# Kernel tuning notes

Hardware: AMD Instinct MI355X
Metric: run time of the kernel (lower is better)

The kernel has to match this reference:

```python
import jax, jax.numpy as jnp
import numpy as np

B, S, D = 4, 2048, 1024
LN_EPS = 1e-3  # keras LayerNormalization default


def setup_inputs() -> dict:
    key = jax.random.key(0)
    ks = jax.random.split(key, 4)
    std = 1.0 / np.sqrt(D)
    return {
        "inputs": jax.random.normal(ks[0], (B, S, D), dtype=jnp.float32),
        "Wq": jax.random.normal(ks[1], (D, D), dtype=jnp.float32) * std,
        "bq": jnp.zeros((D,), jnp.float32),
        "Wk": jax.random.normal(ks[2], (D, D), dtype=jnp.float32) * std,
        "bk": jnp.zeros((D,), jnp.float32),
        "Wv": jax.random.normal(ks[3], (D, D), dtype=jnp.float32) * std,
        "bv": jnp.zeros((D,), jnp.float32),
        "ln_gamma": jnp.ones((D,), jnp.float32),
        "ln_beta": jnp.zeros((D,), jnp.float32),
    }


def reference(inputs, Wq, bq, Wk, bk, Wv, bv, ln_gamma, ln_beta):
    d = inputs.shape[-1]
    scale = jnp.sqrt(jnp.asarray(d, inputs.dtype))
    q = inputs @ Wq + bq          # [B,S,D]
    k = inputs @ Wk + bk
    v = inputs @ Wv + bv
    scores = jnp.einsum("bqd,bkd->bqk", q, k) / scale  # [B,S,S]
    attn = jax.nn.softmax(scores, axis=-1)
    context = jnp.einsum("bqk,bkd->bqd", attn, v)      # [B,S,D]
    resid = context + inputs
    mu = jnp.mean(resid, axis=-1, keepdims=True)
    var = jnp.mean(jnp.square(resid - mu), axis=-1, keepdims=True)
    normed = (resid - mu) * jax.lax.rsqrt(var + LN_EPS)
    return normed * ln_gamma + ln_beta
```

## Files before the change

kernel.cpp:

```cpp
#include <hip/hip_runtime.h>
#include <hip/hip_bf16.h>
#include <cstdint>
#include <cstddef>


typedef unsigned short u16;
using bf16x8 = __attribute__((ext_vector_type(8))) short;
using f32x16 = __attribute__((ext_vector_type(16))) float;

typedef __attribute__((address_space(3))) unsigned int lds_uint;
typedef const __attribute__((address_space(1))) unsigned int glob_uint;

__device__ __forceinline__ float bf2f(u16 h) {
    union { unsigned int u; float f; } c;
    c.u = ((unsigned int)h) << 16;
    return c.f;
}
__device__ __forceinline__ u16 f2bf(float f) {
    union { float f; unsigned int u; } c;
    c.f = f;
    return (u16)((c.u + 0x7fffu + ((c.u >> 16) & 1u)) >> 16);
}
__device__ __forceinline__ void load_lds16(const void* g, void* l) {
    __builtin_amdgcn_global_load_lds((glob_uint*)g, (lds_uint*)l, 16, 0, 0);
}

__device__ __forceinline__ int detect_fp32(const u16* X, int* sflag) {
    const int t = threadIdx.x;
    if (t < 64) {
        bool bad = false, nz = false;
#pragma unroll
        for (int j = 0; j < 4; ++j) {
            float v = bf2f(X[(t * 4 + j) * 2]);
            if (!(fabsf(v) <= 1e9f)) bad = true;
            if (v != 0.f) nz = true;
        }
        unsigned long long ab = __ballot(bad);
        unsigned long long an = __ballot(nz);
        if (t == 0) *sflag = (ab != 0ull || an == 0ull) ? 1 : 0;
    }
    __syncthreads();
    return *sflag;
}

__global__ __launch_bounds__(256) void prep_kernel(
    const void* __restrict__ X, const void* __restrict__ Wq,
    const void* __restrict__ Wk, const void* __restrict__ Wv,
    const void* __restrict__ bq, const void* __restrict__ bk,
    const void* __restrict__ bv, const void* __restrict__ gamma,
    const void* __restrict__ beta,
    u16* __restrict__ Xb, u16* __restrict__ Wt, u16* __restrict__ bias5)
{
    __shared__ u16 tile[64][72];
    __shared__ int sflag;
    const int fp32 = detect_fp32((const u16*)X, &sflag);
    const int t   = threadIdx.x;
    const int blk = blockIdx.x;

    if (blk < 4096) {
        const size_t i = ((size_t)blk * 256 + t) * 8;
        if (fp32) {
            const float* f = (const float*)X;
            float4 a = *(const float4*)(f + i);
            float4 b = *(const float4*)(f + i + 4);
            ushort4 o0, o1;
            o0.x = f2bf(a.x); o0.y = f2bf(a.y); o0.z = f2bf(a.z); o0.w = f2bf(a.w);
            o1.x = f2bf(b.x); o1.y = f2bf(b.y); o1.z = f2bf(b.z); o1.w = f2bf(b.w);
            *(ushort4*)(Xb + i) = o0;
            *(ushort4*)(Xb + i + 4) = o1;
        } else {
            *(uint4*)(Xb + i) = *(const uint4*)((const u16*)X + i);
        }
    } else if (blk < 4864) {
        const int idx = blk - 4096;
        const int k0 = (idx & 15) * 64;
        const int n0 = ((idx >> 4) & 15) * 64;
        const int w  = idx >> 8;
        const void* W = (w == 0) ? Wq : ((w == 1) ? Wk : Wv);
#pragma unroll
        for (int it = 0; it < 2; ++it) {
            int i2 = t + it * 256;
            int r = i2 >> 3;
            int c = (i2 & 7) * 8;
            const size_t off = (size_t)(k0 + r) * 1024 + n0 + c;
            if (fp32) {
                const float* Wf = (const float*)W + off;
                float4 a = *(const float4*)Wf;
                float4 b = *(const float4*)(Wf + 4);
                u16* tp = &tile[r][c];
                tp[0] = f2bf(a.x); tp[1] = f2bf(a.y); tp[2] = f2bf(a.z); tp[3] = f2bf(a.w);
                tp[4] = f2bf(b.x); tp[5] = f2bf(b.y); tp[6] = f2bf(b.z); tp[7] = f2bf(b.w);
            } else {
                *(uint4*)&tile[r][c] = *(const uint4*)((const u16*)W + off);
            }
        }
        __syncthreads();
#pragma unroll
        for (int it = 0; it < 2; ++it) {
            int i2 = t + it * 256;
            int r = i2 >> 3;
            int c = (i2 & 7) * 8;
            union { u16 s[8]; uint4 v; } tmp;
#pragma unroll
            for (int j = 0; j < 8; ++j) tmp.s[j] = tile[c + j][r];
            *(uint4*)(Wt + (size_t)(w * 1024 + n0 + r) * 1024 + k0 + c) = tmp.v;
        }
    } else {
        const int v = blk - 4864;
        const void* srcs[5] = {bq, bk, bv, gamma, beta};
        const void* src = srcs[v];
        u16* d = bias5 + (size_t)v * 1024;
        const int i = t * 4;
        if (fp32) {
            const float* f = (const float*)src;
            ushort4 o;
            o.x = f2bf(f[i]); o.y = f2bf(f[i + 1]);
            o.z = f2bf(f[i + 2]); o.w = f2bf(f[i + 3]);
            *(ushort4*)(d + i) = o;
        } else {
            *(ushort4*)(d + i) = *(const ushort4*)((const u16*)src + i);
        }
    }
}

__global__ __launch_bounds__(256) void transpose_v4_kernel(
    const u16* __restrict__ QKV, u16* __restrict__ Vt4)
{
    __shared__ u16 tile[64][72];
    const int t  = threadIdx.x;
    const int k0 = blockIdx.x * 64;
    const int n0 = blockIdx.y * 64;
    const int b  = blockIdx.z;
    const u16* Vsrc = QKV + (size_t)b * 2048 * 3072 + 2048;
    u16* Vt = Vt4 + (size_t)b * 1024 * 2048;
#pragma unroll
    for (int it = 0; it < 2; ++it) {
        int idx = t + it * 256;
        int r = idx >> 3;
        int c = (idx & 7) * 8;
        *(uint4*)&tile[r][c] = *(const uint4*)(Vsrc + (size_t)(k0 + r) * 3072 + n0 + c);
    }
    __syncthreads();
#pragma unroll
    for (int it = 0; it < 2; ++it) {
        int idx = t + it * 256;
        int r = idx >> 3;
        int c = (idx & 7) * 8;
        union { u16 s[8]; uint4 v; } tmp;
#pragma unroll
        for (int j = 0; j < 8; ++j) tmp.s[j] = tile[c + j][r];
        *(uint4*)(Vt + (size_t)(n0 + r) * 2048 + k0 + c) = tmp.v;
    }
}

template<int EPI, int KSPLIT>
__global__ __launch_bounds__(512, 2) void gemm256r(
    const u16* __restrict__ A, int lda, size_t sA,
    const u16* __restrict__ Bt, int ldb, size_t sB,
    u16* __restrict__ C, int ldc, size_t sC,
    int K, float scale, const u16* __restrict__ bias3)
{
    __shared__ u16 As[2][256 * 64];
    __shared__ u16 Bs[2][256 * 64];

    const int t  = threadIdx.x;
    const int l  = t & 63;
    const int w  = t >> 6;
    const int wm = w >> 2;
    const int wn = w & 3;
    const int m0 = blockIdx.y * 256;
    const int n0 = blockIdx.x * 256;
    const int batch = (int)blockIdx.z >> (KSPLIT - 1);
    const int ks    = (int)blockIdx.z & (KSPLIT - 1);
    A  += (size_t)batch * sA + (size_t)ks * K;
    Bt += (size_t)batch * sB + (size_t)ks * K;
    C  += (size_t)batch * sC + (size_t)ks * 1024;

    const int srow = w * 8 + (l >> 3);
    const int sg   = (l & 7) ^ (l >> 3);
    const u16* Ag = A  + (size_t)(m0 + srow) * lda + sg * 8;
    const u16* Bg = Bt + (size_t)(n0 + srow) * ldb + sg * 8;

    auto stage = [&](int j, int buf) {
        const size_t kb = (size_t)j * 64;
        const u16* ag = Ag + kb;
        const u16* bg = Bg + kb;
        u16* al = &As[buf][w * 512];
        u16* bl = &Bs[buf][w * 512];
#pragma unroll
        for (int i = 0; i < 4; ++i) {
            load_lds16(ag + (size_t)i * 64 * lda, al + i * 4096);
            load_lds16(bg + (size_t)i * 64 * ldb, bl + i * 4096);
        }
    };

    const int lr   = l & 31;
    const int kh   = l >> 5;
    const int keyr = lr & 7;
    const int aoff = (wm * 128 + lr) * 64;
    const int boff = (wn * 64 + lr) * 64;

    f32x16 acc[4][2];
#pragma unroll
    for (int mi = 0; mi < 4; ++mi)
#pragma unroll
        for (int ni = 0; ni < 2; ++ni)
#pragma unroll
            for (int r = 0; r < 16; ++r) acc[mi][ni][r] = 0.f;

    const int NS = K >> 6;

    stage(0, 0);
    stage(1, 1);
    asm volatile("s_waitcnt vmcnt(8)" ::: "memory");
    __builtin_amdgcn_s_barrier();
    asm volatile("" ::: "memory");

    for (int j = 0; j < NS; ++j) {
        const int buf = j & 1;
        const u16* as_ = &As[buf][aoff];
        const u16* bs_ = &Bs[buf][boff];
        bf16x8 a[4][4], b[2][4];
#pragma unroll
        for (int ks2 = 0; ks2 < 2; ++ks2) {
            const int sp = ((ks2 * 2 + kh) ^ keyr) * 8;
#pragma unroll
            for (int mi = 0; mi < 4; ++mi) a[mi][ks2] = *(const bf16x8*)(as_ + mi * 2048 + sp);
#pragma unroll
            for (int ni = 0; ni < 2; ++ni) b[ni][ks2] = *(const bf16x8*)(bs_ + ni * 2048 + sp);
        }
        if (j + 1 < NS) stage(j + 1, buf ^ 1);
        __builtin_amdgcn_s_setprio(1);
#pragma unroll
        for (int ks2 = 0; ks2 < 2; ++ks2)
#pragma unroll
            for (int mi = 0; mi < 4; ++mi)
#pragma unroll
                for (int ni = 0; ni < 2; ++ni)
                    acc[mi][ni] = __builtin_amdgcn_mfma_f32_32x32x16_bf16(
                        a[mi][ks2], b[ni][ks2], acc[mi][ni], 0, 0, 0);
        __builtin_amdgcn_s_setprio(0);
#pragma unroll
        for (int ks2 = 2; ks2 < 4; ++ks2) {
            const int sp = ((ks2 * 2 + kh) ^ keyr) * 8;
#pragma unroll
            for (int mi = 0; mi < 4; ++mi) a[mi][ks2] = *(const bf16x8*)(as_ + mi * 2048 + sp);
#pragma unroll
            for (int ni = 0; ni < 2; ++ni) b[ni][ks2] = *(const bf16x8*)(bs_ + ni * 2048 + sp);
        }
        __builtin_amdgcn_s_setprio(1);
#pragma unroll
        for (int ks2 = 2; ks2 < 4; ++ks2)
#pragma unroll
            for (int mi = 0; mi < 4; ++mi)
#pragma unroll
                for (int ni = 0; ni < 2; ++ni)
                    acc[mi][ni] = __builtin_amdgcn_mfma_f32_32x32x16_bf16(
                        a[mi][ks2], b[ni][ks2], acc[mi][ni], 0, 0, 0);
        __builtin_amdgcn_s_setprio(0);
        if (j + 1 < NS) {
            asm volatile("s_waitcnt vmcnt(0)" ::: "memory");
            __builtin_amdgcn_s_barrier();
            asm volatile("" ::: "memory");
        }
    }

    const int colb = n0 + wn * 64 + lr;
    const int rowb = m0 + wm * 128 + 4 * kh;
#pragma unroll
    for (int mi = 0; mi < 4; ++mi) {
#pragma unroll
        for (int ni = 0; ni < 2; ++ni) {
            const int col = colb + ni * 32;
            const float bias = (EPI == 0) ? bf2f(bias3[col]) : 0.f;
#pragma unroll
            for (int r = 0; r < 16; ++r) {
                const int row = rowb + mi * 32 + (r & 3) + 8 * (r >> 2);
                C[(size_t)row * ldc + col] = f2bf(acc[mi][ni][r] * scale + bias);
            }
        }
    }
}

__global__ __launch_bounds__(256) void softmax_bf16_kernel(u16* __restrict__ S)
{
    const int t = threadIdx.x;
    u16* sp = S + (size_t)blockIdx.x * 2048;
    union { uint4 v; u16 h[8]; } raw;
    raw.v = *(const uint4*)(sp + t * 8);
    float vals[8];
#pragma unroll
    for (int i = 0; i < 8; ++i) vals[i] = bf2f(raw.h[i]);
    float m = vals[0];
#pragma unroll
    for (int i = 1; i < 8; ++i) m = fmaxf(m, vals[i]);
#pragma unroll
    for (int off = 32; off > 0; off >>= 1) m = fmaxf(m, __shfl_xor(m, off));
    __shared__ float red[8];
    const int w = t >> 6, lane = t & 63;
    if (lane == 0) red[w] = m;
    __syncthreads();
    m = fmaxf(fmaxf(red[0], red[1]), fmaxf(red[2], red[3]));
    float e[8], s = 0.f;
#pragma unroll
    for (int i = 0; i < 8; ++i) { e[i] = __expf(vals[i] - m); s += e[i]; }
#pragma unroll
    for (int off = 32; off > 0; off >>= 1) s += __shfl_xor(s, off);
    if (lane == 0) red[4 + w] = s;
    __syncthreads();
    s = red[4] + red[5] + red[6] + red[7];
    const float rinv = 1.f / s;
    union { uint4 v; u16 h[8]; } out;
#pragma unroll
    for (int i = 0; i < 8; ++i) out.h[i] = f2bf(e[i] * rinv);
    *(uint4*)(sp + t * 8) = out.v;
}

__global__ __launch_bounds__(256) void resid_ln_kernel(
    const u16* __restrict__ Ctx, const u16* __restrict__ Xb,
    const u16* __restrict__ gamma, const u16* __restrict__ beta,
    void* __restrict__ Out, const u16* __restrict__ Xraw)
{
    __shared__ int sflag;
    const int fp32 = detect_fp32(Xraw, &sflag);
    const size_t row = blockIdx.x;
    const int t = threadIdx.x;
    ushort4 cv0 = *(const ushort4*)(Ctx + row * 3072 + t * 4);
    ushort4 cv1 = *(const ushort4*)(Ctx + row * 3072 + 1024 + t * 4);
    ushort4 xv  = *(const ushort4*)(Xb + row * 1024 + t * 4);
    float v[4] = {bf2f(cv0.x) + bf2f(cv1.x) + bf2f(xv.x),
                  bf2f(cv0.y) + bf2f(cv1.y) + bf2f(xv.y),
                  bf2f(cv0.z) + bf2f(cv1.z) + bf2f(xv.z),
                  bf2f(cv0.w) + bf2f(cv1.w) + bf2f(xv.w)};
    float s  = v[0] + v[1] + v[2] + v[3];
    float s2 = v[0] * v[0] + v[1] * v[1] + v[2] * v[2] + v[3] * v[3];
#pragma unroll
    for (int off = 32; off > 0; off >>= 1) {
        s  += __shfl_xor(s, off);
        s2 += __shfl_xor(s2, off);
    }
    __shared__ float red[8];
    const int w = t >> 6, lane = t & 63;
    if (lane == 0) { red[w] = s; red[4 + w] = s2; }
    __syncthreads();
    s  = red[0] + red[1] + red[2] + red[3];
    s2 = red[4] + red[5] + red[6] + red[7];
    const float mu  = s * (1.f / 1024.f);
    const float var = s2 * (1.f / 1024.f) - mu * mu;
    const float inv = rsqrtf(var + 1e-3f);
    ushort4 gv = *(const ushort4*)(gamma + t * 4);
    ushort4 bv = *(const ushort4*)(beta + t * 4);
    float o[4];
    o[0] = (v[0] - mu) * inv * bf2f(gv.x) + bf2f(bv.x);
    o[1] = (v[1] - mu) * inv * bf2f(gv.y) + bf2f(bv.y);
    o[2] = (v[2] - mu) * inv * bf2f(gv.z) + bf2f(bv.z);
    o[3] = (v[3] - mu) * inv * bf2f(gv.w) + bf2f(bv.w);
    if (fp32) {
        float4 fo = {o[0], o[1], o[2], o[3]};
        *(float4*)((float*)Out + row * 1024 + t * 4) = fo;
    } else {
        ushort4 bo;
        bo.x = f2bf(o[0]); bo.y = f2bf(o[1]); bo.z = f2bf(o[2]); bo.w = f2bf(o[3]);
        *(ushort4*)((u16*)Out + row * 1024 + t * 4) = bo;
    }
}

extern "C" void kernel_launch(void* const* d_in, const int* in_sizes, int n_in,
                              void* d_out, int out_size, void* d_ws, size_t ws_size,
                              hipStream_t stream)
{
    (void)in_sizes; (void)n_in; (void)out_size; (void)ws_size;
    const void* X     = d_in[0];
    const void* Wq    = d_in[1];
    const void* bq    = d_in[2];
    const void* Wk    = d_in[3];
    const void* bk    = d_in[4];
    const void* Wv    = d_in[5];
    const void* bv    = d_in[6];
    const void* gamma = d_in[7];
    const void* beta  = d_in[8];

    char* ws = (char*)d_ws;
    u16* bias5 = (u16*)(ws + 16);
    u16* Wt    = (u16*)(ws + 16384);
    u16* QKV   = (u16*)(ws + 6307840);
    u16* Xb    = (u16*)(ws + 56639488);
    u16* S4    = (u16*)(ws + 73416704);
    u16* Vt4   = (u16*)(ws + 106971136);

    prep_kernel<<<4869, 256, 0, stream>>>(
        X, Wq, Wk, Wv, bq, bk, bv, gamma, beta, Xb, Wt, bias5);

    gemm256r<0, 1><<<dim3(12, 32, 1), 512, 0, stream>>>(
        Xb, 1024, 0, Wt, 1024, 0, QKV, 3072, 0, 1024, 1.f, bias5);

    gemm256r<1, 1><<<dim3(8, 8, 4), 512, 0, stream>>>(
        QKV, 3072, (size_t)2048 * 3072,
        QKV + 1024, 3072, (size_t)2048 * 3072,
        S4, 2048, (size_t)2048 * 2048, 1024, 0.03125f, nullptr);

    softmax_bf16_kernel<<<8192, 256, 0, stream>>>(S4);

    transpose_v4_kernel<<<dim3(32, 16, 4), 256, 0, stream>>>(QKV, Vt4);

    gemm256r<1, 2><<<dim3(4, 8, 8), 512, 0, stream>>>(
        S4, 2048, (size_t)2048 * 2048,
        Vt4, 2048, (size_t)1024 * 2048,
        QKV, 3072, (size_t)2048 * 3072, 1024, 1.f, nullptr);

    resid_ln_kernel<<<8192, 256, 0, stream>>>(
        QKV, Xb, bias5 + 3 * 1024, bias5 + 4 * 1024, d_out, (const u16*)X);
}
```

Baseline: 287.6 us.

## Fuse V transpose into new projection GEMM and drop transpose kernel

Replaces the 256-tile QKV projection GEMM with a new 128x128 MFMA kernel. It writes Q and K into a compact 2048-wide buffer and computes V already transposed as Wv^T·X^T, so the separate transpose kernel and its extra global round trip go away. Downstream GEMM strides, workspace offsets and the residual/LayerNorm reads are updated to match. It also skips a redundant stage of the second k-slab at the first loop iteration. The new projection kernel is simpler, with no cross-iteration pipelining and scalar 2-byte stores, so it may run the largest GEMM less efficiently than the tuned kernel it replaces.

```diff
diff --git a/kernel.cpp b/kernel.cpp
--- a/kernel.cpp
+++ b/kernel.cpp
@@ -123,33 +123,100 @@
     }
 }
 
-__global__ __launch_bounds__(256) void transpose_v4_kernel(
-    const u16* __restrict__ QKV, u16* __restrict__ Vt4)
-{
-    __shared__ u16 tile[64][72];
-    const int t  = threadIdx.x;
-    const int k0 = blockIdx.x * 64;
-    const int n0 = blockIdx.y * 64;
-    const int b  = blockIdx.z;
-    const u16* Vsrc = QKV + (size_t)b * 2048 * 3072 + 2048;
-    u16* Vt = Vt4 + (size_t)b * 1024 * 2048;
-#pragma unroll
-    for (int it = 0; it < 2; ++it) {
-        int idx = t + it * 256;
-        int r = idx >> 3;
-        int c = (idx & 7) * 8;
-        *(uint4*)&tile[r][c] = *(const uint4*)(Vsrc + (size_t)(k0 + r) * 3072 + n0 + c);
-    }
-    __syncthreads();
-#pragma unroll
-    for (int it = 0; it < 2; ++it) {
-        int idx = t + it * 256;
-        int r = idx >> 3;
-        int c = (idx & 7) * 8;
-        union { u16 s[8]; uint4 v; } tmp;
-#pragma unroll
-        for (int j = 0; j < 8; ++j) tmp.s[j] = tile[c + j][r];
-        *(uint4*)(Vt + (size_t)(n0 + r) * 2048 + k0 + c) = tmp.v;
+__global__ __launch_bounds__(256) void proj_kernel(
+    const u16* __restrict__ Xb, const u16* __restrict__ Wt,
+    u16* __restrict__ QK2, u16* __restrict__ Vt, const u16* __restrict__ bias5)
+{
+    __shared__ u16 As[2][128 * 32];
+    __shared__ u16 Bs[2][128 * 32];
+    const int id   = blockIdx.x;
+    const bool vt  = (id >= 1024);
+    const u16* A;  const u16* Bt;  u16* C;
+    int lda, ldb, ldc, m0, n0;
+    if (!vt) {
+        A = Xb;  lda = 1024;  Bt = Wt;  ldb = 1024;  C = QK2;  ldc = 2048;
+        n0 = (id & 15) * 128;  m0 = (id >> 4) * 128;
+    } else {
+        const int i2 = id - 1024;
+        A = Wt + (size_t)2 * 1024 * 1024;  lda = 1024;
+        Bt = Xb;  ldb = 1024;  C = Vt;  ldc = 8192;
+        n0 = (i2 & 63) * 128;  m0 = (i2 >> 6) * 128;
+    }
+    const int t    = threadIdx.x;
+    const int lane = t & 63;
+    const int w    = t >> 6;
+    const int wr   = w >> 1, wc = w & 1;
+
+    const int srow = lane >> 2;
+    const int skg  = (lane & 3) ^ ((srow >> 1) & 3);
+    const u16* Ag0 = A  + (size_t)(m0 + w * 32 +      srow) * lda + skg * 8;
+    const u16* Ag1 = A  + (size_t)(m0 + w * 32 + 16 + srow) * lda + skg * 8;
+    const u16* Bg0 = Bt + (size_t)(n0 + w * 32 +      srow) * ldb + skg * 8;
+    const u16* Bg1 = Bt + (size_t)(n0 + w * 32 + 16 + srow) * ldb + skg * 8;
+    u16* Al0 = &As[0][(w * 32) * 32];
+    u16* Al1 = &As[1][(w * 32) * 32];
+    u16* Bl0 = &Bs[0][(w * 32) * 32];
+    u16* Bl1 = &Bs[1][(w * 32) * 32];
+
+    f32x16 acc[2][2];
+#pragma unroll
+    for (int mi = 0; mi < 2; ++mi)
+#pragma unroll
+        for (int ni = 0; ni < 2; ++ni)
+#pragma unroll
+            for (int r = 0; r < 16; ++r)
+                acc[mi][ni][r] = 0.f;
+
+    const int ml  = lane & 31;
+    const int kh  = lane >> 5;
+    const int key = (ml >> 1) & 3;
+
+    for (int k0 = 0; k0 < 1024; k0 += 64) {
+        load_lds16(Ag0 + k0,      Al0);
+        load_lds16(Ag1 + k0,      Al0 + 16 * 32);
+        load_lds16(Bg0 + k0,      Bl0);
+        load_lds16(Bg1 + k0,      Bl0 + 16 * 32);
+        load_lds16(Ag0 + k0 + 32, Al1);
+        load_lds16(Ag1 + k0 + 32, Al1 + 16 * 32);
+        load_lds16(Bg0 + k0 + 32, Bl1);
+        load_lds16(Bg1 + k0 + 32, Bl1 + 16 * 32);
+        __syncthreads();
+#pragma unroll
+        for (int slab = 0; slab < 2; ++slab) {
+            const u16* as_ = As[slab];
+            const u16* bs_ = Bs[slab];
+#pragma unroll
+            for (int s = 0; s < 2; ++s) {
+                const int g    = s * 2 + kh;
+                const int slot = (g ^ key) * 8;
+                bf16x8 a0 = *(const bf16x8*)&as_[(wr * 64 +      ml) * 32 + slot];
+                bf16x8 a1 = *(const bf16x8*)&as_[(wr * 64 + 32 + ml) * 32 + slot];
+                bf16x8 b0 = *(const bf16x8*)&bs_[(wc * 64 +      ml) * 32 + slot];
+                bf16x8 b1 = *(const bf16x8*)&bs_[(wc * 64 + 32 + ml) * 32 + slot];
+                acc[0][0] = __builtin_amdgcn_mfma_f32_32x32x16_bf16(a0, b0, acc[0][0], 0, 0, 0);
+                acc[0][1] = __builtin_amdgcn_mfma_f32_32x32x16_bf16(a0, b1, acc[0][1], 0, 0, 0);
+                acc[1][0] = __builtin_amdgcn_mfma_f32_32x32x16_bf16(a1, b0, acc[1][0], 0, 0, 0);
+                acc[1][1] = __builtin_amdgcn_mfma_f32_32x32x16_bf16(a1, b1, acc[1][1], 0, 0, 0);
+            }
+        }
+        __syncthreads();
+    }
+
+    const int colb = n0 + wc * 64 + ml;
+    const int rowb = m0 + wr * 64 + 4 * kh;
+#pragma unroll
+    for (int mi = 0; mi < 2; ++mi) {
+#pragma unroll
+        for (int ni = 0; ni < 2; ++ni) {
+            const int col = colb + ni * 32;
+            const float cbias = vt ? 0.f : bf2f(bias5[col]);
+#pragma unroll
+            for (int r = 0; r < 16; ++r) {
+                const int row = rowb + mi * 32 + (r & 3) + 8 * (r >> 2);
+                const float bias = vt ? bf2f(bias5[2048 + row]) : cbias;
+                C[(size_t)row * ldc + col] = f2bf(acc[mi][ni][r] + bias);
+            }
+        }
     }
 }
 
@@ -229,7 +296,7 @@
 #pragma unroll
             for (int ni = 0; ni < 2; ++ni) b[ni][ks2] = *(const bf16x8*)(bs_ + ni * 2048 + sp);
         }
-        if (j + 1 < NS) stage(j + 1, buf ^ 1);
+        if (j + 1 < NS && j > 0) stage(j + 1, buf ^ 1);
         __builtin_amdgcn_s_setprio(1);
 #pragma unroll
         for (int ks2 = 0; ks2 < 2; ++ks2)
@@ -325,8 +392,8 @@
     const int fp32 = detect_fp32(Xraw, &sflag);
     const size_t row = blockIdx.x;
     const int t = threadIdx.x;
-    ushort4 cv0 = *(const ushort4*)(Ctx + row * 3072 + t * 4);
-    ushort4 cv1 = *(const ushort4*)(Ctx + row * 3072 + 1024 + t * 4);
+    ushort4 cv0 = *(const ushort4*)(Ctx + row * 2048 + t * 4);
+    ushort4 cv1 = *(const ushort4*)(Ctx + row * 2048 + 1024 + t * 4);
     ushort4 xv  = *(const ushort4*)(Xb + row * 1024 + t * 4);
     float v[4] = {bf2f(cv0.x) + bf2f(cv1.x) + bf2f(xv.x),
                   bf2f(cv0.y) + bf2f(cv1.y) + bf2f(xv.y),
@@ -383,31 +450,28 @@
     char* ws = (char*)d_ws;
     u16* bias5 = (u16*)(ws + 16);
     u16* Wt    = (u16*)(ws + 16384);
-    u16* QKV   = (u16*)(ws + 6307840);
-    u16* Xb    = (u16*)(ws + 56639488);
-    u16* S4    = (u16*)(ws + 73416704);
-    u16* Vt4   = (u16*)(ws + 106971136);
+    u16* QK2   = (u16*)(ws + 6307840);
+    u16* Xb    = (u16*)(ws + 39862272);
+    u16* S4    = (u16*)(ws + 56639488);
+    u16* Vt    = (u16*)(ws + 90193920);
 
     prep_kernel<<<4869, 256, 0, stream>>>(
         X, Wq, Wk, Wv, bq, bk, bv, gamma, beta, Xb, Wt, bias5);
 
-    gemm256r<0, 1><<<dim3(12, 32, 1), 512, 0, stream>>>(
-        Xb, 1024, 0, Wt, 1024, 0, QKV, 3072, 0, 1024, 1.f, bias5);
+    proj_kernel<<<1536, 256, 0, stream>>>(Xb, Wt, QK2, Vt, bias5);
 
     gemm256r<1, 1><<<dim3(8, 8, 4), 512, 0, stream>>>(
-        QKV, 3072, (size_t)2048 * 3072,
-        QKV + 1024, 3072, (size_t)2048 * 3072,
+        QK2, 2048, (size_t)2048 * 2048,
+        QK2 + 1024, 2048, (size_t)2048 * 2048,
         S4, 2048, (size_t)2048 * 2048, 1024, 0.03125f, nullptr);
 
     softmax_bf16_kernel<<<8192, 256, 0, stream>>>(S4);
-
-    transpose_v4_kernel<<<dim3(32, 16, 4), 256, 0, stream>>>(QKV, Vt4);
 
     gemm256r<1, 2><<<dim3(4, 8, 8), 512, 0, stream>>>(
         S4, 2048, (size_t)2048 * 2048,
-        Vt4, 2048, (size_t)1024 * 2048,
-        QKV, 3072, (size_t)2048 * 3072, 1024, 1.f, nullptr);
+        Vt, 8192, (size_t)2048,
+        QK2, 2048, (size_t)2048 * 2048, 1024, 1.f, nullptr);
 
     resid_ln_kernel<<<8192, 256, 0, stream>>>(
-        QKV, Xb, bias5 + 3 * 1024, bias5 + 4 * 1024, d_out, (const u16*)X);
-}
+        QK2, Xb, bias5 + 3 * 1024, bias5 + 4 * 1024, d_out, (const u16*)X);
+}
```

Result: faster. 280.2 us (-2.6%).
